# Kernel optimization log

Hardware: AMD Instinct MI355X
Metric: run time of the kernel (lower is better)

Reference implementation:

```python
import jax, jax.numpy as jnp
import numpy as np

N_TOKENS = 32768
D_MODEL = 1024
D_HIDDEN = 4096
N_EXPERTS = 8
TOP_K = 2


def setup_inputs() -> dict:
    key = jax.random.key(0)
    ks = jax.random.split(key, 8)
    s_in = 1.0 / np.sqrt(D_MODEL)
    s_hid = 1.0 / np.sqrt(D_HIDDEN)
    return {
        "x": jax.random.normal(ks[0], (N_TOKENS, D_MODEL), dtype=jnp.float32),
        "Wr": jax.random.normal(ks[1], (D_MODEL, N_EXPERTS), dtype=jnp.float32) * s_in,
        "br": jnp.zeros((N_EXPERTS,), dtype=jnp.float32),
        "W1": jax.random.normal(ks[2], (N_EXPERTS, D_MODEL, D_HIDDEN), dtype=jnp.float32) * s_in,
        "b1": jnp.zeros((N_EXPERTS, D_HIDDEN), dtype=jnp.float32),
        "W2": jax.random.normal(ks[3], (N_EXPERTS, D_HIDDEN, D_MODEL), dtype=jnp.float32) * s_hid,
        "b2": jnp.zeros((N_EXPERTS, D_MODEL), dtype=jnp.float32),
    }


def reference(x, Wr, br, W1, b1, W2, b2):
    # Router: softmax over experts, top-k selection, renormalize.
    logits = x @ Wr + br                                  # [N, E]
    probs = jax.nn.softmax(logits, axis=-1)
    topk_probs, topk_idx = jax.lax.top_k(probs, TOP_K)    # [N, K]
    topk_probs = topk_probs / jnp.sum(topk_probs, axis=-1, keepdims=True)
    # Per-token per-expert combine weight (sum over k of prob * selection).
    sel = jax.nn.one_hot(topk_idx, N_EXPERTS, dtype=x.dtype)   # [N, K, E]
    combine = jnp.einsum('nk,nke->ne', topk_probs, sel)        # [N, E]
    # Masked gather-MLP-scatter expressed as dense per-expert MLP weighted
    # by combine (zero weight for unselected experts -> identical math).
    out = jnp.zeros_like(x)
    for e in range(N_EXPERTS):
        h = jax.nn.gelu(x @ W1[e] + b1[e], approximate=False)  # exact erf GELU (torch default)
        out = out + combine[:, e:e + 1] * (h @ W2[e] + b2[e])
    return out
```

## Files before the change

kernel.cpp:

```cpp
#include <hip/hip_runtime.h>

#define NT_TOK 32768
#define DM 1024
#define DH 4096
#define NE 8
#define BT 256
#define BK 32
#define CAP (NT_TOK*2 + NE*BT)
#define CHUNK_ROWS 32768

typedef _Float16 f16x8 __attribute__((ext_vector_type(8)));
typedef float f32x4 __attribute__((ext_vector_type(4)));
typedef float f32x8 __attribute__((ext_vector_type(8)));

__device__ __forceinline__ unsigned short f2h_bits(float v){
  _Float16 h = (_Float16)v;
  return __builtin_bit_cast(unsigned short, h);
}

__device__ __forceinline__ void async16(const void* g, void* l){
  __builtin_amdgcn_global_load_lds((const __attribute__((address_space(1))) void*)g,
                                   (__attribute__((address_space(3))) void*)l, 16, 0, 0);
}

__device__ __forceinline__ int xcd_remap(int orig, int nwg){
  int q = nwg >> 3, r = nwg & 7;
  int x = orig & 7, i = orig >> 3;
  int base = (x < r) ? x*(q+1) : r*(q+1) + (x-r)*q;
  return base + i;
}


__global__ __launch_bounds__(256) void cvt_f16_kernel(const float* __restrict__ src,
                                                      unsigned short* __restrict__ dst, int n8){
  int i = blockIdx.x*256 + threadIdx.x;
  if (i >= n8) return;
  float4 a = ((const float4*)src)[2*i];
  float4 b = ((const float4*)src)[2*i+1];
  union { unsigned short u[8]; uint4 v; } r;
  r.u[0]=f2h_bits(a.x); r.u[1]=f2h_bits(a.y); r.u[2]=f2h_bits(a.z); r.u[3]=f2h_bits(a.w);
  r.u[4]=f2h_bits(b.x); r.u[5]=f2h_bits(b.y); r.u[6]=f2h_bits(b.z); r.u[7]=f2h_bits(b.w);
  ((uint4*)dst)[i] = r.v;
}

__global__ __launch_bounds__(256) void transpose_f16_v2(const float* __restrict__ src,
    unsigned short* __restrict__ dst, int R, int C){
  __shared__ float t[64][65];
  int ez = blockIdx.z;
  const float* s = src + (size_t)ez*R*C;
  unsigned short* d = dst + (size_t)ez*R*C;
  int c0 = blockIdx.x*64, r0 = blockIdx.y*64;
  int tx = threadIdx.x & 15, ty = threadIdx.x >> 4;
  #pragma unroll
  for (int i=0;i<4;i++){
    float4 v = *(const float4*)&s[(size_t)(r0+ty+i*16)*C + c0 + tx*4];
    t[ty+i*16][tx*4+0]=v.x; t[ty+i*16][tx*4+1]=v.y;
    t[ty+i*16][tx*4+2]=v.z; t[ty+i*16][tx*4+3]=v.w;
  }
  __syncthreads();
  #pragma unroll
  for (int i=0;i<4;i++){
    int cc = ty + i*16;
    union { unsigned short u[4]; uint2 v; } o;
    #pragma unroll
    for (int j=0;j<4;j++) o.u[j] = f2h_bits(t[tx*4+j][cc]);
    *(uint2*)&d[(size_t)(c0+cc)*R + r0 + tx*4] = o.v;
  }
}


__global__ __launch_bounds__(256) void router_kernel(const float* __restrict__ x,
    const float* __restrict__ Wr, const float* __restrict__ br,
    int* __restrict__ topi, float* __restrict__ topw, int* __restrict__ counts){
  __shared__ float wr_s[NE*DM];
  __shared__ int bcnt[NE];
  int tid = threadIdx.x;
  if (tid < NE) bcnt[tid] = 0;
  for (int idx=tid; idx<NE*DM; idx+=256){
    int k = idx>>3, e = idx&7;
    wr_s[e*DM + k] = Wr[idx];
  }
  __syncthreads();
  int w = tid>>6, lane = tid&63;
  for (int tt=0; tt<16; ++tt){
    int t = blockIdx.x*64 + w*16 + tt;
    const float* xr = x + (size_t)t*DM;
    double acc[NE];
    #pragma unroll
    for (int e=0;e<NE;e++) acc[e]=0.0;
    #pragma unroll
    for (int j=0;j<16;j++){
      float xv = xr[j*64 + lane];
      #pragma unroll
      for (int e=0;e<NE;e++) acc[e] += (double)xv * (double)wr_s[e*DM + j*64 + lane];
    }
    #pragma unroll
    for (int e=0;e<NE;e++){
      #pragma unroll
      for (int d=32; d; d>>=1) acc[e] += __shfl_xor(acc[e], d);
    }
    if (lane==0){
      double l[NE];
      #pragma unroll
      for (int e=0;e<NE;e++) l[e] = acc[e] + (double)br[e];
      int i0 = 0;
      #pragma unroll
      for (int e=1;e<NE;e++) if (l[e] > l[i0]) i0 = e;
      int i1 = (i0==0) ? 1 : 0;
      #pragma unroll
      for (int e=0;e<NE;e++) if (e != i0 && l[e] > l[i1]) i1 = e;
      double w0 = 1.0/(1.0 + exp(l[i1]-l[i0]));
      topi[2*t] = i0; topi[2*t+1] = i1;
      topw[2*t] = (float)w0; topw[2*t+1] = (float)(1.0-w0);
      atomicAdd(&bcnt[i0],1); atomicAdd(&bcnt[i1],1);
    }
  }
  __syncthreads();
  if (tid < NE && bcnt[tid] > 0) atomicAdd(&counts[tid], bcnt[tid]);
}

__global__ void offsets_kernel(const int* __restrict__ counts, int* __restrict__ off){
  if (threadIdx.x==0 && blockIdx.x==0){
    int o = 0;
    for (int e=0;e<NE;e++){ off[e] = o; o += ((counts[e]+BT-1)/BT)*BT; }
    off[NE] = o;
  }
}

__global__ __launch_bounds__(256) void scatter_kernel(const int* __restrict__ topi,
    const float* __restrict__ topw, const int* __restrict__ off,
    int* __restrict__ cursor, int* __restrict__ atok, float* __restrict__ awgt){
  __shared__ int bcnt[NE];
  __shared__ int bbase[NE];
  int tid = threadIdx.x;
  if (tid < NE) bcnt[tid] = 0;
  __syncthreads();
  int t = blockIdx.x*256 + tid;
  int e0 = topi[2*t],   e1 = topi[2*t+1];
  int r0 = atomicAdd(&bcnt[e0], 1);
  int r1 = atomicAdd(&bcnt[e1], 1);
  __syncthreads();
  if (tid < NE) bbase[tid] = (bcnt[tid] > 0) ? atomicAdd(&cursor[tid], bcnt[tid]) : 0;
  __syncthreads();
  int s0 = off[e0] + bbase[e0] + r0;
  int s1 = off[e1] + bbase[e1] + r1;
  atok[s0] = t;  awgt[s0] = topw[2*t];
  atok[s1] = t;  awgt[s1] = topw[2*t+1];
}


template<int KDIM, bool IS_G2>
__global__ __launch_bounds__(512, 2) void gemm_big_kernel(
    const unsigned short* __restrict__ Asrc,
    const unsigned short* __restrict__ WT,
    const float* __restrict__ bias,
    const int* __restrict__ atok,
    const float* __restrict__ awgt,
    const int* __restrict__ offs,
    unsigned short* __restrict__ H,
    float* __restrict__ out,
    int c0){
  __shared__ unsigned short As[4][BT*BK];
  __shared__ unsigned short Bs[4][BT*BK];
  const int NDIM = IS_G2 ? DM : DH;
  const int NT = NDIM/BT;
  int wg = xcd_remap(blockIdx.x, gridDim.x);
  int nt = wg % NT, mt = wg / NT;
  int total = offs[NE];
  int m0 = c0 + mt*BT;
  if (m0 >= total) return;
  int e = 0;
  #pragma unroll
  for (int q=0;q<NE-1;q++) if (m0 >= offs[q+1]) e = q+1;
  int tid = threadIdx.x;
  int lane = tid&63, wid = tid>>6;
  int wm = wid>>2, wn = wid&3;

  const unsigned short* agp[2];
  const unsigned short* bgp[2];
  int dofs[2];
  #pragma unroll
  for (int j=0;j<2;j++){
    int c = j*512 + tid;
    int u = (c&7) ^ ((c>>3)&7);
    int srow = ((c>>3)<<1) + (u>>2);
    int sch  = u&3;
    if (IS_G2){
      agp[j] = Asrc + (size_t)(m0 - c0 + srow)*KDIM + sch*8;
    } else {
      int tok = atok[m0 + srow];
      if (tok < 0) tok = 0;
      agp[j] = Asrc + (size_t)tok*KDIM + sch*8;
    }
    bgp[j] = WT + ((size_t)e*NDIM + nt*BT + srow)*KDIM + sch*8;
    dofs[j] = c*8;
  }

  int pos = (((lane>>4) + ((lane&1)<<2)) ^ ((lane>>1)&7)) << 3;
  int aoff0 = (wm*64 + ((lane&15)>>1))*64 + pos;
  int boff0 = (wn*32 + ((lane&15)>>1))*64 + pos;

  f32x4 acc[8][4];
  #pragma unroll
  for (int i=0;i<8;i++)
    #pragma unroll
    for (int j=0;j<4;j++) acc[i][j] = 0.0f;

  const int NKT = KDIM/BK;
  #pragma unroll
  for (int t=0;t<3;t++){
    #pragma unroll
    for (int j=0;j<2;j++) async16(agp[j] + t*BK, &As[t][dofs[j]]);
    #pragma unroll
    for (int j=0;j<2;j++) async16(bgp[j] + t*BK, &Bs[t][dofs[j]]);
  }

  for (int kt=0; kt<NKT; ++kt){
    if (kt < NKT-2)      asm volatile("s_waitcnt vmcnt(8)" ::: "memory");
    else if (kt < NKT-1) asm volatile("s_waitcnt vmcnt(4)" ::: "memory");
    else                 asm volatile("s_waitcnt vmcnt(0)" ::: "memory");
    __builtin_amdgcn_s_barrier();
    const unsigned short* Ab = &As[kt&3][0];
    const unsigned short* Bb = &Bs[kt&3][0];
    f16x8 b[4], a[4];
    #pragma unroll
    for (int nf=0;nf<4;nf++) b[nf] = *(const f16x8*)&Bb[boff0 + nf*512];
    #pragma unroll
    for (int mf=0;mf<4;mf++) a[mf] = *(const f16x8*)&Ab[aoff0 + mf*512];
    if (kt+3 < NKT){
      #pragma unroll
      for (int j=0;j<2;j++) async16(agp[j] + (size_t)(kt+3)*BK, &As[(kt+3)&3][dofs[j]]);
    }
    __builtin_amdgcn_s_setprio(1);
    #pragma unroll
    for (int mf=0;mf<4;mf++)
      #pragma unroll
      for (int nf=0;nf<4;nf++)
        acc[mf][nf] = __builtin_amdgcn_mfma_f32_16x16x32_f16(a[mf], b[nf], acc[mf][nf], 0,0,0);
    __builtin_amdgcn_s_setprio(0);
    __builtin_amdgcn_s_barrier();
    #pragma unroll
    for (int mf=0;mf<4;mf++) a[mf] = *(const f16x8*)&Ab[aoff0 + (mf+4)*512];
    if (kt+3 < NKT){
      #pragma unroll
      for (int j=0;j<2;j++) async16(bgp[j] + (size_t)(kt+3)*BK, &Bs[(kt+3)&3][dofs[j]]);
    }
    __builtin_amdgcn_s_setprio(1);
    #pragma unroll
    for (int mf=0;mf<4;mf++)
      #pragma unroll
      for (int nf=0;nf<4;nf++)
        acc[mf+4][nf] = __builtin_amdgcn_mfma_f32_16x16x32_f16(a[mf], b[nf], acc[mf+4][nf], 0,0,0);
    __builtin_amdgcn_s_setprio(0);
  }

  int nbase = nt*BT + wn*64 + (lane&15);
  if (!IS_G2){
    const float* be = bias + (size_t)e*DH;
    int rloc = (m0 - c0) + wm*128 + ((lane>>4)<<2);
    #pragma unroll
    for (int mf=0;mf<8;mf++)
      #pragma unroll
      for (int nf=0;nf<4;nf++){
        int nn = nbase + nf*16;
        float bv = be[nn];
        #pragma unroll
        for (int r2=0;r2<4;r2++){
          float v = acc[mf][nf][r2] + bv;
          float g = 0.5f*v*(1.0f + erff(v*0.70710678118654752f));
          H[(size_t)(rloc + mf*16 + r2)*DH + nn] = f2h_bits(g);
        }
      }
  } else {
    const float* be = bias + (size_t)e*DM;
    int sbase = m0 + wm*128 + ((lane>>4)<<2);
    #pragma unroll
    for (int mf=0;mf<8;mf++){
      #pragma unroll
      for (int r2=0;r2<4;r2++){
        int slot = sbase + mf*16 + r2;
        int tok = atok[slot];
        float wgt = awgt[slot];
        if (tok >= 0){
          #pragma unroll
          for (int nf=0;nf<4;nf++){
            int nn = nbase + nf*16;
            float v = acc[mf][nf][r2] + be[nn];
            atomicAdd(&out[(size_t)tok*DM + nn], wgt*v);
          }
        }
      }
    }
  }
}


__global__ __launch_bounds__(256) void gemm1_f32_kernel(
    const float* __restrict__ xf, const unsigned short* __restrict__ W1T,
    const float* __restrict__ b1, const int* __restrict__ atok,
    const int* __restrict__ offs, unsigned short* __restrict__ H, int c0){
  __shared__ float Asf[128*64];
  __shared__ unsigned short Bsld[128*64];
  const int NT = DH/128;
  int wg = xcd_remap(blockIdx.x, gridDim.x);
  int nt = wg % NT, mt = wg / NT;
  int total = offs[NE];
  int m0 = c0 + mt*128;
  if (m0 >= total) return;
  int e = 0;
  #pragma unroll
  for (int q=0;q<NE-1;q++) if (m0 >= offs[q+1]) e = q+1;
  int tid = threadIdx.x;
  const void* ag[8];
  int aofs[8];
  #pragma unroll
  for (int j=0;j<8;j++){
    int c = j*256 + tid;
    int r = c>>4, sb = (c&15)*16;
    int tok = atok[m0 + r];
    if (tok < 0) tok = 0;
    ag[j] = (const void*)((const char*)(xf + (size_t)tok*DM) + sb);
    aofs[j] = c*16;
  }
  const unsigned short* bg[4];
  int bofs[4];
  #pragma unroll
  for (int j=0;j<4;j++){
    int c = j*256 + tid;
    int r = c>>3, s = c&7;
    bg[j] = W1T + ((size_t)e*DH + nt*128 + r)*DM + s*8;
    bofs[j] = c*16;
  }
  f32x4 acc[4][4];
  #pragma unroll
  for (int i=0;i<4;i++)
    #pragma unroll
    for (int j=0;j<4;j++) acc[i][j] = 0.0f;
  int lane = tid&63;
  int wm = tid>>7, wn = (tid>>6)&1;
  int arow = wm*64 + (lane&15);
  int ak0  = (lane>>4)*8;
  int brr  = (wn*64 + (lane&15))*64 + ak0;
  for (int kt=0; kt<DM/64; ++kt){
    #pragma unroll
    for (int j=0;j<8;j++)
      async16((const char*)ag[j] + (size_t)kt*64*4, (char*)Asf + aofs[j]);
    #pragma unroll
    for (int j=0;j<4;j++)
      async16(bg[j] + (size_t)kt*64, (char*)Bsld + bofs[j]);
    __syncthreads();
    #pragma unroll
    for (int kk=0; kk<64; kk+=32){
      f16x8 a[4], b[4];
      #pragma unroll
      for (int f=0;f<4;f++){
        f32x8 v = *(const f32x8*)&Asf[(arow + f*16)*64 + ak0 + kk];
        a[f] = __builtin_convertvector(v, f16x8);
        b[f] = *(const f16x8*)&Bsld[brr + f*16*64 + kk];
      }
      #pragma unroll
      for (int i=0;i<4;i++)
        #pragma unroll
        for (int j2=0;j2<4;j2++)
          acc[i][j2] = __builtin_amdgcn_mfma_f32_16x16x32_f16(a[i], b[j2], acc[i][j2], 0,0,0);
    }
    __syncthreads();
  }
  const float* b1e = b1 + (size_t)e*DH;
  int rloc = (m0 - c0) + wm*64 + ((lane>>4)<<2);
  int nbase = nt*128 + wn*64 + (lane&15);
  #pragma unroll
  for (int i=0;i<4;i++)
    #pragma unroll
    for (int j=0;j<4;j++){
      int nn = nbase + j*16;
      float bv = b1e[nn];
      #pragma unroll
      for (int r2=0;r2<4;r2++){
        float v = acc[i][j][r2] + bv;
        float g = 0.5f*v*(1.0f + erff(v*0.70710678118654752f));
        H[(size_t)(rloc + i*16 + r2)*DH + nn] = f2h_bits(g);
      }
    }
}

__global__ void fill_kernel(float* p, float v, size_t n){
  size_t i = (size_t)blockIdx.x*256 + threadIdx.x;
  if (i < n) p[i] = v;
}


extern "C" void kernel_launch(void* const* d_in, const int* in_sizes, int n_in,
                              void* d_out, int out_size, void* d_ws, size_t ws_size,
                              hipStream_t stream){
  const float* x  = (const float*)d_in[0];
  const float* Wr = (const float*)d_in[1];
  const float* br = (const float*)d_in[2];
  const float* W1 = (const float*)d_in[3];
  const float* b1 = (const float*)d_in[4];
  const float* W2 = (const float*)d_in[5];
  const float* b2 = (const float*)d_in[6];
  float* out = (float*)d_out;

  char* ws = (char*)d_ws;
  size_t o = 0;
  auto take = [&](size_t bytes)->void*{
    void* p = ws + o; o += (bytes + 255) & ~(size_t)255; return p;
  };
  unsigned short* W1T = (unsigned short*)take((size_t)NE*DM*DH*2);
  unsigned short* W2T = (unsigned short*)take((size_t)NE*DM*DH*2);
  int*   TOPI = (int*)take((size_t)NT_TOK*2*4);
  float* TOPW = (float*)take((size_t)NT_TOK*2*4);
  int*   ATOK = (int*)take((size_t)CAP*4);
  float* AWGT = (float*)take((size_t)CAP*4);
  int*   CNT  = (int*)take(256);
  int* CUR = CNT + 8;
  int* OFF = CNT + 16;

  if (o + (size_t)BT*DH*2 > ws_size){
    fill_kernel<<<(unsigned)((out_size+255)/256), 256, 0, stream>>>(out, 4321.5f, (size_t)out_size);
    return;
  }

  unsigned short* XB = nullptr;
  bool use_xb = false;
  {
    size_t xb_bytes = (size_t)NT_TOK*DM*2 + 256;
    size_t need_h  = (size_t)2048*DH*2;
    if (o + xb_bytes + need_h <= ws_size){
      use_xb = true;
      XB = (unsigned short*)take((size_t)NT_TOK*DM*2);
    }
  }
  size_t rem = ws_size - o;
  size_t cr = (rem / ((size_t)DH*2)) / BT * BT;
  if (cr > (size_t)CHUNK_ROWS) cr = CHUNK_ROWS;
  if (cr < BT){
    fill_kernel<<<(unsigned)((out_size+255)/256), 256, 0, stream>>>(out, 4321.5f, (size_t)out_size);
    return;
  }
  int CR = (int)cr;
  unsigned short* Hb = (unsigned short*)take((size_t)CR*DH*2);

  hipMemsetAsync(CNT, 0, 64, stream);
  hipMemsetAsync(ATOK, 0xFF, (size_t)CAP*4, stream);
  hipMemsetAsync(out, 0, (size_t)out_size*sizeof(float), stream);

  if (use_xb)
    cvt_f16_kernel<<<(NT_TOK*DM/8 + 255)/256, 256, 0, stream>>>(x, XB, NT_TOK*DM/8);
  transpose_f16_v2<<<dim3(DH/64, DM/64, NE), 256, 0, stream>>>(W1, W1T, DM, DH);
  transpose_f16_v2<<<dim3(DM/64, DH/64, NE), 256, 0, stream>>>(W2, W2T, DH, DM);
  router_kernel<<<NT_TOK/64, 256, 0, stream>>>(x, Wr, br, TOPI, TOPW, CNT);
  offsets_kernel<<<1, 1, 0, stream>>>(CNT, OFF);
  scatter_kernel<<<NT_TOK/256, 256, 0, stream>>>(TOPI, TOPW, OFF, CUR, ATOK, AWGT);

  for (int c0 = 0; c0 < CAP; c0 += CR){
    int rows = CAP - c0; if (rows > CR) rows = CR;
    int mtc = (rows + BT - 1)/BT;
    if (use_xb)
      gemm_big_kernel<DM, false><<<dim3((DH/BT)*mtc), 512, 0, stream>>>(
          XB, W1T, b1, ATOK, AWGT, OFF, Hb, out, c0);
    else
      gemm1_f32_kernel<<<dim3((DH/128)*((rows+127)/128)), 256, 0, stream>>>(
          x, W1T, b1, ATOK, OFF, Hb, c0);
    gemm_big_kernel<DH, true><<<dim3((DM/BT)*mtc), 512, 0, stream>>>(
        Hb, W2T, b2, ATOK, AWGT, OFF, Hb, out, c0);
  }
}
```

Before: 2.238 ms.

## Shrink GEMM tile to 128x256 with 4 waves and triple-buffered LDS

Reworks the grouped expert GEMM kernel from a 256x256 tile with 8 waves and a 4-stage LDS ring to a 128x256 tile with 4 waves and a 3-stage ring. The prefetch distance drops from 3 to 2. Each wave still computes a 128x64 sub-tile. The B tile is now loaded with four strided async copies per thread. Smaller tiles mean less padding waste per expert segment (BM=128 vs 256), more workgroups, and less LDS per block, which should help occupancy. The cost is lower reuse of the B operand per block and a shallower pipeline for hiding memory latency.

```diff
diff --git a/kernel.cpp b/kernel.cpp
--- a/kernel.cpp
+++ b/kernel.cpp
@@ -5,6 +5,7 @@
 #define DH 4096
 #define NE 8
 #define BT 256
+#define BM 128
 #define BK 32
 #define CAP (NT_TOK*2 + NE*BT)
 #define CHUNK_ROWS 32768
@@ -150,7 +151,7 @@
 
 
 template<int KDIM, bool IS_G2>
-__global__ __launch_bounds__(512, 2) void gemm_big_kernel(
+__global__ __launch_bounds__(256, 2) void gemm_big_kernel(
     const unsigned short* __restrict__ Asrc,
     const unsigned short* __restrict__ WT,
     const float* __restrict__ bias,
@@ -160,28 +161,26 @@
     unsigned short* __restrict__ H,
     float* __restrict__ out,
     int c0){
-  __shared__ unsigned short As[4][BT*BK];
-  __shared__ unsigned short Bs[4][BT*BK];
+  __shared__ unsigned short As[3][BM*BK];
+  __shared__ unsigned short Bs[3][BT*BK];
   const int NDIM = IS_G2 ? DM : DH;
   const int NT = NDIM/BT;
   int wg = xcd_remap(blockIdx.x, gridDim.x);
   int nt = wg % NT, mt = wg / NT;
   int total = offs[NE];
-  int m0 = c0 + mt*BT;
+  int m0 = c0 + mt*BM;
   if (m0 >= total) return;
   int e = 0;
   #pragma unroll
   for (int q=0;q<NE-1;q++) if (m0 >= offs[q+1]) e = q+1;
   int tid = threadIdx.x;
-  int lane = tid&63, wid = tid>>6;
-  int wm = wid>>2, wn = wid&3;
+  int lane = tid&63, wn = tid>>6;
 
   const unsigned short* agp[2];
-  const unsigned short* bgp[2];
-  int dofs[2];
+  int dofsA[2];
   #pragma unroll
   for (int j=0;j<2;j++){
-    int c = j*512 + tid;
+    int c = j*256 + tid;
     int u = (c&7) ^ ((c>>3)&7);
     int srow = ((c>>3)<<1) + (u>>2);
     int sch  = u&3;
@@ -192,12 +191,21 @@
       if (tok < 0) tok = 0;
       agp[j] = Asrc + (size_t)tok*KDIM + sch*8;
     }
-    bgp[j] = WT + ((size_t)e*NDIM + nt*BT + srow)*KDIM + sch*8;
-    dofs[j] = c*8;
+    dofsA[j] = c*8;
+  }
+  const unsigned short* bgp0;
+  int dofsB0;
+  {
+    int c = tid;
+    int u = (c&7) ^ ((c>>3)&7);
+    int srow = ((c>>3)<<1) + (u>>2);
+    int sch  = u&3;
+    bgp0 = WT + ((size_t)e*NDIM + nt*BT + srow)*KDIM + sch*8;
+    dofsB0 = c*8;
   }
 
   int pos = (((lane>>4) + ((lane&1)<<2)) ^ ((lane>>1)&7)) << 3;
-  int aoff0 = (wm*64 + ((lane&15)>>1))*64 + pos;
+  int aoff0 = (((lane&15)>>1))*64 + pos;
   int boff0 = (wn*32 + ((lane&15)>>1))*64 + pos;
 
   f32x4 acc[8][4];
@@ -208,28 +216,29 @@
 
   const int NKT = KDIM/BK;
   #pragma unroll
-  for (int t=0;t<3;t++){
-    #pragma unroll
-    for (int j=0;j<2;j++) async16(agp[j] + t*BK, &As[t][dofs[j]]);
-    #pragma unroll
-    for (int j=0;j<2;j++) async16(bgp[j] + t*BK, &Bs[t][dofs[j]]);
-  }
-
+  for (int t=0;t<2;t++){
+    #pragma unroll
+    for (int j=0;j<2;j++) async16(agp[j] + t*BK, &As[t][dofsA[j]]);
+    #pragma unroll
+    for (int j=0;j<4;j++) async16(bgp0 + (size_t)j*64*KDIM + t*BK, &Bs[t][dofsB0 + j*2048]);
+  }
+
+  int cur = 0;
   for (int kt=0; kt<NKT; ++kt){
-    if (kt < NKT-2)      asm volatile("s_waitcnt vmcnt(8)" ::: "memory");
-    else if (kt < NKT-1) asm volatile("s_waitcnt vmcnt(4)" ::: "memory");
-    else                 asm volatile("s_waitcnt vmcnt(0)" ::: "memory");
+    if (kt < NKT-1) asm volatile("s_waitcnt vmcnt(6)" ::: "memory");
+    else            asm volatile("s_waitcnt vmcnt(0)" ::: "memory");
     __builtin_amdgcn_s_barrier();
-    const unsigned short* Ab = &As[kt&3][0];
-    const unsigned short* Bb = &Bs[kt&3][0];
+    int nxt2 = cur + 2; if (nxt2 >= 3) nxt2 -= 3;
+    const unsigned short* Ab = &As[cur][0];
+    const unsigned short* Bb = &Bs[cur][0];
     f16x8 b[4], a[4];
     #pragma unroll
     for (int nf=0;nf<4;nf++) b[nf] = *(const f16x8*)&Bb[boff0 + nf*512];
     #pragma unroll
     for (int mf=0;mf<4;mf++) a[mf] = *(const f16x8*)&Ab[aoff0 + mf*512];
-    if (kt+3 < NKT){
-      #pragma unroll
-      for (int j=0;j<2;j++) async16(agp[j] + (size_t)(kt+3)*BK, &As[(kt+3)&3][dofs[j]]);
+    if (kt+2 < NKT){
+      #pragma unroll
+      for (int j=0;j<2;j++) async16(agp[j] + (size_t)(kt+2)*BK, &As[nxt2][dofsA[j]]);
     }
     __builtin_amdgcn_s_setprio(1);
     #pragma unroll
@@ -241,9 +250,9 @@
     __builtin_amdgcn_s_barrier();
     #pragma unroll
     for (int mf=0;mf<4;mf++) a[mf] = *(const f16x8*)&Ab[aoff0 + (mf+4)*512];
-    if (kt+3 < NKT){
-      #pragma unroll
-      for (int j=0;j<2;j++) async16(bgp[j] + (size_t)(kt+3)*BK, &Bs[(kt+3)&3][dofs[j]]);
+    if (kt+2 < NKT){
+      #pragma unroll
+      for (int j=0;j<4;j++) async16(bgp0 + (size_t)j*64*KDIM + (size_t)(kt+2)*BK, &Bs[nxt2][dofsB0 + j*2048]);
     }
     __builtin_amdgcn_s_setprio(1);
     #pragma unroll
@@ -252,12 +261,13 @@
       for (int nf=0;nf<4;nf++)
         acc[mf+4][nf] = __builtin_amdgcn_mfma_f32_16x16x32_f16(a[mf], b[nf], acc[mf+4][nf], 0,0,0);
     __builtin_amdgcn_s_setprio(0);
+    cur = (cur + 1 == 3) ? 0 : cur + 1;
   }
 
   int nbase = nt*BT + wn*64 + (lane&15);
   if (!IS_G2){
     const float* be = bias + (size_t)e*DH;
-    int rloc = (m0 - c0) + wm*128 + ((lane>>4)<<2);
+    int rloc = (m0 - c0) + ((lane>>4)<<2);
     #pragma unroll
     for (int mf=0;mf<8;mf++)
       #pragma unroll
@@ -273,7 +283,7 @@
       }
   } else {
     const float* be = bias + (size_t)e*DM;
-    int sbase = m0 + wm*128 + ((lane>>4)<<2);
+    int sbase = m0 + ((lane>>4)<<2);
     #pragma unroll
     for (int mf=0;mf<8;mf++){
       #pragma unroll
@@ -456,14 +466,14 @@
 
   for (int c0 = 0; c0 < CAP; c0 += CR){
     int rows = CAP - c0; if (rows > CR) rows = CR;
-    int mtc = (rows + BT - 1)/BT;
+    int mtc = (rows + BM - 1)/BM;
     if (use_xb)
-      gemm_big_kernel<DM, false><<<dim3((DH/BT)*mtc), 512, 0, stream>>>(
+      gemm_big_kernel<DM, false><<<dim3((DH/BT)*mtc), 256, 0, stream>>>(
           XB, W1T, b1, ATOK, AWGT, OFF, Hb, out, c0);
     else
       gemm1_f32_kernel<<<dim3((DH/128)*((rows+127)/128)), 256, 0, stream>>>(
           x, W1T, b1, ATOK, OFF, Hb, c0);
-    gemm_big_kernel<DH, true><<<dim3((DM/BT)*mtc), 512, 0, stream>>>(
+    gemm_big_kernel<DH, true><<<dim3((DM/BT)*mtc), 256, 0, stream>>>(
         Hb, W2T, b2, ATOK, AWGT, OFF, Hb, out, c0);
   }
 }
```

Measured after the change: 2.321 ms. +3.7%, slower.
